# Performance work log

Hardware: AMD Instinct MI355X
Metric: run time of the kernel (lower is better)

The kernel has to match this reference:

```python
import jax, jax.numpy as jnp
import numpy as np

B, D, DIN, M, H = 64, 512, 512, 32, 64
DSQ = D * D

def layer_norm(x, g, b, eps=1e-5):
    mu = jnp.mean(x, axis=-1, keepdims=True)
    var = jnp.mean((x - mu) ** 2, axis=-1, keepdims=True)
    return (x - mu) * jax.lax.rsqrt(var + eps) * g + b

def setup_inputs() -> dict:
    key = jax.random.key(0)
    ks = jax.random.split(key, 12)
    sa = 1.0 / np.sqrt(M + 2 * H)   # SuperLinear 1 init scale
    sb = 1.0 / np.sqrt(H + 2)       # SuperLinear 2 init scale
    return {
        "x": jax.random.normal(ks[0], (B, DIN), jnp.float32),
        "pre_activations": jax.random.normal(ks[1], (B, D, M), jnp.float32) * 0.5,
        "post_activations": jax.random.normal(ks[2], (B, D, M), jnp.float32) * 0.5,
        "decay_alpha": jax.random.normal(ks[3], (B, DSQ), jnp.float32) * 0.1,
        "decay_beta": jnp.ones((B, DSQ), jnp.float32),
        "Wp": jax.random.normal(ks[4], (D, DIN + D), jnp.float32) * 0.02,
        "bp": jnp.zeros((D,), jnp.float32),
        "weights_fixed": jax.random.normal(ks[5], (D, D), jnp.float32) * 0.02,
        "ln_syn_g": jnp.ones((D,), jnp.float32),
        "ln_syn_b": jnp.zeros((D,), jnp.float32),
        "w1a": jax.random.uniform(ks[6], (M, 2 * H, D), jnp.float32, -sa, sa),
        "b1a": jnp.zeros((1, D, 2 * H), jnp.float32),
        "ln_nlm_g": jnp.ones((H,), jnp.float32),
        "ln_nlm_b": jnp.zeros((H,), jnp.float32),
        "w1b": jax.random.uniform(ks[7], (H, 2, D), jnp.float32, -sb, sb),
        "b1b": jnp.zeros((1, D, 2), jnp.float32),
        "decay_params": jax.random.uniform(ks[8], (DSQ,), jnp.float32) * 2.0,
        "ln_sync_g": jnp.ones((DSQ,), jnp.float32),
        "ln_sync_b": jnp.zeros((DSQ,), jnp.float32),
    }

def reference(x, pre_activations, post_activations, decay_alpha, decay_beta,
              Wp, bp, weights_fixed, ln_syn_g, ln_syn_b,
              w1a, b1a, ln_nlm_g, ln_nlm_b, w1b, b1b,
              decay_params, ln_sync_g, ln_sync_b):
    # ---- PlasticLinear synapses (no plastic weights, bias=False, layernorm=True)
    activated_state = post_activations[:, :, -1]                  # [B, D]
    inp = jnp.concatenate([x, activated_state], axis=-1)          # [B, DIN+D]
    y = inp @ Wp.T + bp                                           # LazyLinear proj -> [B, D]
    wn = weights_fixed / jnp.linalg.norm(weights_fixed)           # Frobenius-normalized (same per sample)
    state = layer_norm(y @ wn, ln_syn_g, ln_syn_b)                # [B, D]
    # ---- update memory trace
    st = jnp.concatenate([pre_activations[:, :, -M:][:, :, 1:], state[:, :, None]], axis=-1)  # [B, D, M]
    # ---- NLMs: SuperLinear -> GLU -> LN -> SuperLinear -> GLU
    h = jnp.einsum('bdm,mhd->bdh', st, w1a) + b1a                 # [B, D, 2H]
    a, g = jnp.split(h, 2, axis=-1)
    h = a * jax.nn.sigmoid(g)                                     # [B, D, H]
    h = layer_norm(h, ln_nlm_g, ln_nlm_b)
    o = jnp.einsum('bdm,mhd->bdh', h, w1b) + b1b                  # [B, D, 2]
    a2, g2 = jnp.split(o, 2, axis=-1)
    act_new = (a2 * jax.nn.sigmoid(g2))[:, :, 0]                  # [B, D]
    # ---- Synchronizer
    dw = jnp.exp(-jnp.clip(decay_params, 0.0, 15.0))              # [DSQ]
    pairwise = (act_new[:, :, None] * act_new[:, None, :]).reshape(act_new.shape[0], DSQ)
    da = dw ** 2 * decay_alpha + pairwise
    db = dw ** 2 * decay_beta + 1.0
    sync = layer_norm(da / jnp.sqrt(db), ln_sync_g, ln_sync_b)    # [B, DSQ]
    return sync
```

## Files before the change

### kernel.cpp

```cpp
#include <hip/hip_runtime.h>
#include <hip/hip_bf16.h>

#define BB 64
#define DD 512
#define DINN 512
#define MM 32
#define HH 64
#define DSQ (DD*DD)

typedef unsigned short u16;
typedef unsigned int u32;

__device__ float g_state[BB * DD];
__device__ float g_act[BB * DD];
__device__ float g_y[BB * DD];
__device__ float g_t[BB * DD];
__device__ float g_wnt[DD * DD];
__device__ float g_w1at[(size_t)MM * 2 * HH * DD];
__device__ float g_part[BB * 64 * 2];
__device__ float g_wfpart[256];
__device__ u16   g_rbf[(size_t)BB * DSQ];

__device__ __forceinline__ float wave_sum(float v) {
#pragma unroll
  for (int m = 32; m; m >>= 1) v += __shfl_xor(v, m);
  return v;
}
__device__ __forceinline__ float sigmoidf_(float x) {
  return 1.f / (1.f + __expf(-x));
}
__device__ __forceinline__ float bf2f(u32 u) { return __uint_as_float(u << 16); }
__device__ __forceinline__ u16 f2bf(float v) {
  __hip_bfloat16 h = __float2bfloat16(v);
  return *reinterpret_cast<u16*>(&h);
}
__device__ __forceinline__ u32 pack2(float a, float b) {
  return (u32)f2bf(a) | ((u32)f2bf(b) << 16);
}
__device__ __forceinline__ float r_elem(float p, float al, float be, float pw) {
  float c  = fminf(fmaxf(p, 0.f), 15.f);
  float w2 = __expf(-2.f * c);
  return (w2 * al + pw) * rsqrtf(w2 * be + 1.f);
}

__global__ __launch_bounds__(256) void k_twf(const float* __restrict__ Wfix) {
  __shared__ float tile[32][33];
  int c0 = blockIdx.x * 32;
  int r0 = blockIdx.y * 32;
  int tx = threadIdx.x & 31, ty = threadIdx.x >> 5;
  float s = 0.f;
#pragma unroll
  for (int i = 0; i < 32; i += 8) {
    float v = Wfix[(size_t)(r0 + ty + i) * DD + c0 + tx];
    tile[ty + i][tx] = v;
    s = fmaf(v, v, s);
  }
  __syncthreads();
#pragma unroll
  for (int i = 0; i < 32; i += 8)
    g_wnt[(size_t)(c0 + ty + i) * DD + r0 + tx] = tile[tx][ty + i];
  s = wave_sum(s);
  __shared__ float red[4];
  int wv = threadIdx.x >> 6, ln = threadIdx.x & 63;
  if (ln == 0) red[wv] = s;
  __syncthreads();
  if (threadIdx.x == 0)
    g_wfpart[blockIdx.y * 16 + blockIdx.x] = red[0] + red[1] + red[2] + red[3];
}

__global__ __launch_bounds__(256) void k_transpose(const float* __restrict__ A) {
  __shared__ float tile[32][33];
  int c0 = blockIdx.x * 32;
  int r0 = blockIdx.y * 32;
  int tx = threadIdx.x & 31, ty = threadIdx.x >> 5;
#pragma unroll
  for (int i = 0; i < 32; i += 8)
    tile[ty + i][tx] = A[(size_t)(r0 + ty + i) * DD + c0 + tx];
  __syncthreads();
#pragma unroll
  for (int i = 0; i < 32; i += 8)
    g_w1at[(size_t)(c0 + ty + i) * 4096 + r0 + tx] = tile[tx][ty + i];
}

__global__ __launch_bounds__(256) void k_y(
    const float* __restrict__ x, const float* __restrict__ post,
    const float* __restrict__ Wp, const float* __restrict__ bp) {
  __shared__ __align__(16) float inp[DINN + DD];
  const int b = blockIdx.y;
  const int d0 = blockIdx.x * 64;
  for (int i = threadIdx.x; i < DD; i += 256) {
    inp[i]        = x[(size_t)b * DINN + i];
    inp[DINN + i] = post[((size_t)b * DD + i) * MM + (MM - 1)];
  }
  __syncthreads();
  const int wv = threadIdx.x >> 6, ln = threadIdx.x & 63;
  const float4* i4 = (const float4*)inp;
#pragma unroll 4
  for (int j = 0; j < 16; ++j) {
    const int d = d0 + wv * 16 + j;
    const float4* wr = (const float4*)(Wp + (size_t)d * (DINN + DD));
    float a = 0.f;
#pragma unroll
    for (int it = 0; it < 4; ++it) {
      float4 w = wr[it * 64 + ln];
      float4 iv = i4[it * 64 + ln];
      a = fmaf(iv.x, w.x, a); a = fmaf(iv.y, w.y, a);
      a = fmaf(iv.z, w.z, a); a = fmaf(iv.w, w.w, a);
    }
    a = wave_sum(a);
    if (ln == 0) g_y[b * DD + d] = a + bp[d];
  }
}

__global__ __launch_bounds__(256) void k_t(const float* __restrict__ dummy) {
  __shared__ __align__(16) float yld[DD];
  __shared__ float red[4];
  __shared__ float wf2s;
  const int b = blockIdx.y;
  const int d0 = blockIdx.x * 64;
  for (int i = threadIdx.x; i < DD; i += 256) yld[i] = g_y[b * DD + i];
  {
    float w = g_wfpart[threadIdx.x];
    w = wave_sum(w);
    int wv = threadIdx.x >> 6, ln = threadIdx.x & 63;
    if (ln == 0) red[wv] = w;
    __syncthreads();
    if (threadIdx.x == 0) wf2s = red[0] + red[1] + red[2] + red[3];
    __syncthreads();
  }
  const float scale = rsqrtf(wf2s);
  const int wv = threadIdx.x >> 6, ln = threadIdx.x & 63;
  const float4* y4 = (const float4*)yld;
#pragma unroll 4
  for (int j = 0; j < 16; ++j) {
    const int d = d0 + wv * 16 + j;
    const float4* wr = (const float4*)(g_wnt + (size_t)d * DD);
    float a = 0.f;
#pragma unroll
    for (int it = 0; it < 2; ++it) {
      float4 w = wr[it * 64 + ln];
      float4 yv = y4[it * 64 + ln];
      a = fmaf(yv.x, w.x, a); a = fmaf(yv.y, w.y, a);
      a = fmaf(yv.z, w.z, a); a = fmaf(yv.w, w.w, a);
    }
    a = wave_sum(a);
    if (ln == 0) g_t[b * DD + d] = a * scale;
  }
}

__global__ __launch_bounds__(512) void k_ln(const float* __restrict__ lng,
                                            const float* __restrict__ lnb) {
  __shared__ float red[16];
  const int b = blockIdx.x;
  const int t = threadIdx.x;
  float tv = g_t[b * DD + t];
  int wave = t >> 6, lane = t & 63;
  float v = wave_sum(tv);
  if (lane == 0) red[wave] = v;
  __syncthreads();
  float tot = 0.f;
#pragma unroll
  for (int i = 0; i < 8; ++i) tot += red[i];
  float mu = tot * (1.f / 512.f);
  float dv = tv - mu;
  float v2 = wave_sum(dv * dv);
  if (lane == 0) red[8 + wave] = v2;
  __syncthreads();
  float tot2 = 0.f;
#pragma unroll
  for (int i = 0; i < 8; ++i) tot2 += red[8 + i];
  float rstd = rsqrtf(tot2 * (1.f / 512.f) + 1e-5f);
  g_state[b * DD + t] = dv * rstd * lng[t] + lnb[t];
}

__global__ __launch_bounds__(256) void k_act(
    const float* __restrict__ pre, const float* __restrict__ b1a,
    const float* __restrict__ lng, const float* __restrict__ lnb,
    const float* __restrict__ w1b, const float* __restrict__ b1b) {
  __shared__ float W[MM * 2 * HH];
  __shared__ float st[BB][MM + 1];
  __shared__ float wb[2 * HH];
  __shared__ float ba[2 * HH];
  const int d = blockIdx.x;
  const int t = threadIdx.x;
  {
    const float* Wg = g_w1at + (size_t)d * (MM * 2 * HH);
    for (int i = t; i < MM * 2 * HH; i += 256) W[i] = Wg[i];
  }
  if (t < 128) {
    wb[t] = w1b[(size_t)t * DD + d];
    ba[t] = b1a[(size_t)d * 128 + t];
  }
  {
    int b = t >> 2, c = t & 3;
    const size_t pb = (size_t)b * DD * MM + (size_t)d * MM;
    float sv = g_state[b * DD + d];
#pragma unroll
    for (int mm2 = c * 8; mm2 < c * 8 + 8; ++mm2)
      st[b][mm2] = (mm2 < MM - 1) ? pre[pb + mm2 + 1] : sv;
  }
  __syncthreads();
  const int wave = t >> 6, lane = t & 63;
  const float g_ln = lng[lane], b_ln = lnb[lane];
  const float wb0 = wb[2 * lane], wb1 = wb[2 * lane + 1];
  const float baa = ba[lane], bag = ba[64 + lane];
  const float bb0 = b1b[2 * d], bb1 = b1b[2 * d + 1];
  for (int b = wave; b < BB; b += 4) {
    float a = baa, g = bag;
#pragma unroll
    for (int m = 0; m < MM; ++m) {
      float s = st[b][m];
      a = fmaf(s, W[m * 128 + lane], a);
      g = fmaf(s, W[m * 128 + 64 + lane], g);
    }
    float hg = a * sigmoidf_(g);
    float mu = wave_sum(hg) * (1.f / 64.f);
    float dv = hg - mu;
    float var = wave_sum(dv * dv) * (1.f / 64.f);
    float hn = dv * rsqrtf(var + 1e-5f) * g_ln + b_ln;
    float o0 = wave_sum(hn * wb0) + bb0;
    float o1 = wave_sum(hn * wb1) + bb1;
    if (lane == 0) g_act[b * DD + d] = o0 * sigmoidf_(o1);
  }
}

__global__ __launch_bounds__(256) void k_r(
    const float* __restrict__ alpha, const float* __restrict__ beta,
    const float* __restrict__ dp) {
  const int b   = blockIdx.x >> 6;
  const int blk = blockIdx.x & 63;
  const float* arow = g_act + b * DD;
  const size_t rowbase = (size_t)b * DSQ;
  float s = 0.f, ss = 0.f;
#pragma unroll
  for (int it = 0; it < 2; ++it) {
    const int off = blk * 4096 + it * 2048 + threadIdx.x * 8;
    const float4 a0 = *(const float4*)(alpha + rowbase + off);
    const float4 a1 = *(const float4*)(alpha + rowbase + off + 4);
    const float4 be0 = *(const float4*)(beta + rowbase + off);
    const float4 be1 = *(const float4*)(beta + rowbase + off + 4);
    const float4 p0 = *(const float4*)(dp + off);
    const float4 p1 = *(const float4*)(dp + off + 4);
    const float ai = arow[off >> 9];
    const int j = off & 511;
    const float4 aj0 = *(const float4*)(arow + j);
    const float4 aj1 = *(const float4*)(arow + j + 4);
    float av[8]  = {a0.x, a0.y, a0.z, a0.w, a1.x, a1.y, a1.z, a1.w};
    float bv[8]  = {be0.x, be0.y, be0.z, be0.w, be1.x, be1.y, be1.z, be1.w};
    float pv[8]  = {p0.x, p0.y, p0.z, p0.w, p1.x, p1.y, p1.z, p1.w};
    float ajv[8] = {aj0.x, aj0.y, aj0.z, aj0.w, aj1.x, aj1.y, aj1.z, aj1.w};
    float rv[8];
#pragma unroll
    for (int e = 0; e < 8; ++e) {
      float r = r_elem(pv[e], av[e], bv[e], ai * ajv[e]);
      rv[e] = r;
      s += r;
      ss = fmaf(r, r, ss);
    }
    uint4 pk;
    pk.x = pack2(rv[0], rv[1]);
    pk.y = pack2(rv[2], rv[3]);
    pk.z = pack2(rv[4], rv[5]);
    pk.w = pack2(rv[6], rv[7]);
    *reinterpret_cast<uint4*>(g_rbf + rowbase + off) = pk;
  }
  s = wave_sum(s); ss = wave_sum(ss);
  __shared__ float rs[4], rss[4];
  int wave = threadIdx.x >> 6, lane = threadIdx.x & 63;
  if (lane == 0) { rs[wave] = s; rss[wave] = ss; }
  __syncthreads();
  if (threadIdx.x == 0) {
    g_part[(b * 64 + blk) * 2]     = rs[0] + rs[1] + rs[2] + rs[3];
    g_part[(b * 64 + blk) * 2 + 1] = rss[0] + rss[1] + rss[2] + rss[3];
  }
}

__global__ __launch_bounds__(256) void k_out(
    const float* __restrict__ g, const float* __restrict__ bn,
    float* __restrict__ out) {
  const int b   = blockIdx.x >> 6;
  const int blk = blockIdx.x & 63;
  __shared__ float sm[2];
  {
    const int t = threadIdx.x;
    if (t < 64) {
      float s  = g_part[(b * 64 + t) * 2];
      float ss = g_part[(b * 64 + t) * 2 + 1];
      s = wave_sum(s); ss = wave_sum(ss);
      if (t == 0) {
        float mean = s * (1.f / (float)DSQ);
        float var  = ss * (1.f / (float)DSQ) - mean * mean;
        sm[0] = mean;
        sm[1] = rsqrtf(fmaxf(var, 0.f) + 1e-5f);
      }
    }
  }
  __syncthreads();
  const float mean = sm[0];
  const float rstd = sm[1];
  const size_t rowbase = (size_t)b * DSQ;
#pragma unroll
  for (int it = 0; it < 2; ++it) {
    const int off = blk * 4096 + it * 2048 + threadIdx.x * 8;
    const uint4 rp = *(const uint4*)(g_rbf + rowbase + off);
    const float4 g0 = *(const float4*)(g + off);
    const float4 g1 = *(const float4*)(g + off + 4);
    const float4 n0 = *(const float4*)(bn + off);
    const float4 n1 = *(const float4*)(bn + off + 4);
    float rv[8] = {bf2f(rp.x & 0xffff), bf2f(rp.x >> 16),
                   bf2f(rp.y & 0xffff), bf2f(rp.y >> 16),
                   bf2f(rp.z & 0xffff), bf2f(rp.z >> 16),
                   bf2f(rp.w & 0xffff), bf2f(rp.w >> 16)};
    float gv[8] = {g0.x, g0.y, g0.z, g0.w, g1.x, g1.y, g1.z, g1.w};
    float nv[8] = {n0.x, n0.y, n0.z, n0.w, n1.x, n1.y, n1.z, n1.w};
    float v[8];
#pragma unroll
    for (int e = 0; e < 8; ++e)
      v[e] = (rv[e] - mean) * rstd * gv[e] + nv[e];
    *(float4*)(out + rowbase + off)     = make_float4(v[0], v[1], v[2], v[3]);
    *(float4*)(out + rowbase + off + 4) = make_float4(v[4], v[5], v[6], v[7]);
  }
}

extern "C" void kernel_launch(void* const* d_in, const int* in_sizes, int n_in,
                              void* d_out, int out_size, void* d_ws, size_t ws_size,
                              hipStream_t stream) {
  const float* x      = (const float*)d_in[0];
  const float* pre    = (const float*)d_in[1];
  const float* post   = (const float*)d_in[2];
  const float* dalpha = (const float*)d_in[3];
  const float* dbeta  = (const float*)d_in[4];
  const float* Wp     = (const float*)d_in[5];
  const float* bp     = (const float*)d_in[6];
  const float* wfix   = (const float*)d_in[7];
  const float* lnsg   = (const float*)d_in[8];
  const float* lnsb   = (const float*)d_in[9];
  const float* w1a    = (const float*)d_in[10];
  const float* b1a    = (const float*)d_in[11];
  const float* lnng   = (const float*)d_in[12];
  const float* lnnb   = (const float*)d_in[13];
  const float* w1b    = (const float*)d_in[14];
  const float* b1b    = (const float*)d_in[15];
  const float* dparam = (const float*)d_in[16];
  const float* lncg   = (const float*)d_in[17];
  const float* lncb   = (const float*)d_in[18];
  float* out = (float*)d_out;

  k_twf<<<dim3(16, 16), 256, 0, stream>>>(wfix);
  k_y<<<dim3(8, 64), 256, 0, stream>>>(x, post, Wp, bp);
  k_t<<<dim3(8, 64), 256, 0, stream>>>(nullptr);
  k_ln<<<64, 512, 0, stream>>>(lnsg, lnsb);
  k_transpose<<<dim3(16, 128), 256, 0, stream>>>(w1a);
  k_act<<<512, 256, 0, stream>>>(pre, b1a, lnng, lnnb, w1b, b1b);
  k_r<<<4096, 256, 0, stream>>>(dalpha, dbeta, dparam);
  k_out<<<4096, 256, 0, stream>>>(lncg, lncb, out);
}
```

Measured before the change: 292.1 us.

## Fuse sync compute and layernorm into one kernel with LDS staging and grid barrier

Merges the elementwise sync-compute kernel and the layernorm output kernel into one kernel. Each of 512 blocks keeps its 32K bf16 intermediate values in LDS instead of writing them to global memory and reading them back. Per-row statistics are combined across the 8 blocks of a row through a global atomic counter and spin-wait. This removes the global intermediate round trip and one launch. It relies on all 512 blocks being resident at once (64KB LDS each) to avoid deadlock, and the per-row counter is reset inside the first kernel.

```diff
diff --git a/kernel.cpp b/kernel.cpp
--- a/kernel.cpp
+++ b/kernel.cpp
@@ -19,7 +19,7 @@
 __device__ float g_w1at[(size_t)MM * 2 * HH * DD];
 __device__ float g_part[BB * 64 * 2];
 __device__ float g_wfpart[256];
-__device__ u16   g_rbf[(size_t)BB * DSQ];
+__device__ int   g_sync[BB * 16];
 
 __device__ __forceinline__ float wave_sum(float v) {
 #pragma unroll
@@ -45,6 +45,8 @@
 
 __global__ __launch_bounds__(256) void k_twf(const float* __restrict__ Wfix) {
   __shared__ float tile[32][33];
+  if (blockIdx.x == 0 && blockIdx.y == 0 && threadIdx.x < BB)
+    g_sync[threadIdx.x * 16] = 0;
   int c0 = blockIdx.x * 32;
   int r0 = blockIdx.y * 32;
   int tx = threadIdx.x & 31, ty = threadIdx.x >> 5;
@@ -224,25 +226,33 @@
   }
 }
 
-__global__ __launch_bounds__(256) void k_r(
+__global__ __launch_bounds__(512, 4) void k_rout(
     const float* __restrict__ alpha, const float* __restrict__ beta,
-    const float* __restrict__ dp) {
-  const int b   = blockIdx.x >> 6;
-  const int blk = blockIdx.x & 63;
-  const float* arow = g_act + b * DD;
-  const size_t rowbase = (size_t)b * DSQ;
+    const float* __restrict__ dp, const float* __restrict__ lng,
+    const float* __restrict__ lnb, float* __restrict__ out) {
+  __shared__ __align__(16) u16 rl[32768];
+  __shared__ float red[16];
+  __shared__ float sm[2];
+  const int row = blockIdx.x >> 3;
+  const int q   = blockIdx.x & 7;
+  const int tid = threadIdx.x;
+  const float* __restrict__ arow = g_act + row * DD;
+  const size_t rbase = (size_t)row * DSQ;
+  const int qbase = q * 32768;
+
   float s = 0.f, ss = 0.f;
-#pragma unroll
-  for (int it = 0; it < 2; ++it) {
-    const int off = blk * 4096 + it * 2048 + threadIdx.x * 8;
-    const float4 a0 = *(const float4*)(alpha + rowbase + off);
-    const float4 a1 = *(const float4*)(alpha + rowbase + off + 4);
-    const float4 be0 = *(const float4*)(beta + rowbase + off);
-    const float4 be1 = *(const float4*)(beta + rowbase + off + 4);
-    const float4 p0 = *(const float4*)(dp + off);
-    const float4 p1 = *(const float4*)(dp + off + 4);
-    const float ai = arow[off >> 9];
-    const int j = off & 511;
+#pragma unroll 2
+  for (int it = 0; it < 8; ++it) {
+    const int loff = it * 4096 + tid * 8;
+    const int goff = qbase + loff;
+    const float4 a0  = *(const float4*)(alpha + rbase + goff);
+    const float4 a1  = *(const float4*)(alpha + rbase + goff + 4);
+    const float4 be0 = *(const float4*)(beta + rbase + goff);
+    const float4 be1 = *(const float4*)(beta + rbase + goff + 4);
+    const float4 p0  = *(const float4*)(dp + goff);
+    const float4 p1  = *(const float4*)(dp + goff + 4);
+    const float ai = arow[goff >> 9];
+    const int j = goff & 511;
     const float4 aj0 = *(const float4*)(arow + j);
     const float4 aj1 = *(const float4*)(arow + j + 4);
     float av[8]  = {a0.x, a0.y, a0.z, a0.w, a1.x, a1.y, a1.z, a1.w};
@@ -262,51 +272,51 @@
     pk.y = pack2(rv[2], rv[3]);
     pk.z = pack2(rv[4], rv[5]);
     pk.w = pack2(rv[6], rv[7]);
-    *reinterpret_cast<uint4*>(g_rbf + rowbase + off) = pk;
+    *reinterpret_cast<uint4*>(rl + loff) = pk;
   }
   s = wave_sum(s); ss = wave_sum(ss);
-  __shared__ float rs[4], rss[4];
-  int wave = threadIdx.x >> 6, lane = threadIdx.x & 63;
-  if (lane == 0) { rs[wave] = s; rss[wave] = ss; }
-  __syncthreads();
-  if (threadIdx.x == 0) {
-    g_part[(b * 64 + blk) * 2]     = rs[0] + rs[1] + rs[2] + rs[3];
-    g_part[(b * 64 + blk) * 2 + 1] = rss[0] + rss[1] + rss[2] + rss[3];
-  }
-}
-
-__global__ __launch_bounds__(256) void k_out(
-    const float* __restrict__ g, const float* __restrict__ bn,
-    float* __restrict__ out) {
-  const int b   = blockIdx.x >> 6;
-  const int blk = blockIdx.x & 63;
-  __shared__ float sm[2];
   {
-    const int t = threadIdx.x;
-    if (t < 64) {
-      float s  = g_part[(b * 64 + t) * 2];
-      float ss = g_part[(b * 64 + t) * 2 + 1];
-      s = wave_sum(s); ss = wave_sum(ss);
-      if (t == 0) {
-        float mean = s * (1.f / (float)DSQ);
-        float var  = ss * (1.f / (float)DSQ) - mean * mean;
-        sm[0] = mean;
-        sm[1] = rsqrtf(fmaxf(var, 0.f) + 1e-5f);
-      }
-    }
+    const int wv = tid >> 6, ln = tid & 63;
+    if (ln == 0) { red[wv] = s; red[8 + wv] = ss; }
+  }
+  __syncthreads();
+
+  if (tid == 0) {
+    float ps = 0.f, pss = 0.f;
+#pragma unroll
+    for (int i = 0; i < 8; ++i) { ps += red[i]; pss += red[8 + i]; }
+    g_part[(row * 8 + q) * 2]     = ps;
+    g_part[(row * 8 + q) * 2 + 1] = pss;
+    __threadfence();
+    atomicAdd(&g_sync[row * 16], 1);
+    while (__hip_atomic_load(&g_sync[row * 16], __ATOMIC_ACQUIRE,
+                             __HIP_MEMORY_SCOPE_AGENT) < 8) { }
+    float S = 0.f, SS = 0.f;
+#pragma unroll
+    for (int i = 0; i < 8; ++i) {
+      S  += __hip_atomic_load(&g_part[(row * 8 + i) * 2], __ATOMIC_RELAXED,
+                              __HIP_MEMORY_SCOPE_AGENT);
+      SS += __hip_atomic_load(&g_part[(row * 8 + i) * 2 + 1], __ATOMIC_RELAXED,
+                              __HIP_MEMORY_SCOPE_AGENT);
+    }
+    const float mean = S * (1.f / (float)DSQ);
+    const float var  = SS * (1.f / (float)DSQ) - mean * mean;
+    sm[0] = mean;
+    sm[1] = rsqrtf(fmaxf(var, 0.f) + 1e-5f);
   }
   __syncthreads();
   const float mean = sm[0];
   const float rstd = sm[1];
-  const size_t rowbase = (size_t)b * DSQ;
-#pragma unroll
-  for (int it = 0; it < 2; ++it) {
-    const int off = blk * 4096 + it * 2048 + threadIdx.x * 8;
-    const uint4 rp = *(const uint4*)(g_rbf + rowbase + off);
-    const float4 g0 = *(const float4*)(g + off);
-    const float4 g1 = *(const float4*)(g + off + 4);
-    const float4 n0 = *(const float4*)(bn + off);
-    const float4 n1 = *(const float4*)(bn + off + 4);
+
+#pragma unroll 2
+  for (int it = 0; it < 8; ++it) {
+    const int loff = it * 4096 + tid * 8;
+    const int goff = qbase + loff;
+    const uint4 rp = *reinterpret_cast<const uint4*>(rl + loff);
+    const float4 g0 = *(const float4*)(lng + goff);
+    const float4 g1 = *(const float4*)(lng + goff + 4);
+    const float4 n0 = *(const float4*)(lnb + goff);
+    const float4 n1 = *(const float4*)(lnb + goff + 4);
     float rv[8] = {bf2f(rp.x & 0xffff), bf2f(rp.x >> 16),
                    bf2f(rp.y & 0xffff), bf2f(rp.y >> 16),
                    bf2f(rp.z & 0xffff), bf2f(rp.z >> 16),
@@ -317,8 +327,8 @@
 #pragma unroll
     for (int e = 0; e < 8; ++e)
       v[e] = (rv[e] - mean) * rstd * gv[e] + nv[e];
-    *(float4*)(out + rowbase + off)     = make_float4(v[0], v[1], v[2], v[3]);
-    *(float4*)(out + rowbase + off + 4) = make_float4(v[4], v[5], v[6], v[7]);
+    *(float4*)(out + rbase + goff)     = make_float4(v[0], v[1], v[2], v[3]);
+    *(float4*)(out + rbase + goff + 4) = make_float4(v[4], v[5], v[6], v[7]);
   }
 }
 
@@ -352,6 +362,5 @@
   k_ln<<<64, 512, 0, stream>>>(lnsg, lnsb);
   k_transpose<<<dim3(16, 128), 256, 0, stream>>>(w1a);
   k_act<<<512, 256, 0, stream>>>(pre, b1a, lnng, lnnb, w1b, b1b);
-  k_r<<<4096, 256, 0, stream>>>(dalpha, dbeta, dparam);
-  k_out<<<4096, 256, 0, stream>>>(lncg, lncb, out);
-}
+  k_rout<<<512, 512, 0, stream>>>(dalpha, dbeta, dparam, lncg, lncb, out);
+}
```

New measurement: 370.1 us. 1.27x slower.
